# Optimization experiments

Measured on AMD Instinct MI355X. Metric: run time of the kernel, lower is better.

## Reference

```python
import jax, jax.numpy as jnp
import numpy as np

HEAD_DIM = 128
N_HEADS = 16
N_KV_HEADS = 4
N_REP = N_HEADS // N_KV_HEADS


def _rope(x, cos, sin):
    # x: [B, S, Hk, D]; cos/sin: [S, D/2]
    xr = x.reshape(*x.shape[:-1], -1, 2)
    x0, x1 = xr[..., 0], xr[..., 1]
    c = cos[None, :, None, :]
    s = sin[None, :, None, :]
    o0 = x0 * c - x1 * s
    o1 = x0 * s + x1 * c
    return jnp.stack([o0, o1], axis=-1).reshape(x.shape)


def setup_inputs() -> dict:
    key = jax.random.key(0)
    ks = jax.random.split(key, 7)
    B, S, DIM = 2, 1024, 2048
    KV_DIM = HEAD_DIM * N_KV_HEADS
    x = jax.random.normal(ks[0], (B, S, DIM), dtype=jnp.float32)
    # rotary angles like LLaMA: freqs = 1/10000^(2i/D)
    inv_freq = 1.0 / (10000.0 ** (np.arange(0, HEAD_DIM, 2, dtype=np.float32) / HEAD_DIM))
    ang = np.arange(S, dtype=np.float32)[:, None] * inv_freq[None, :]  # [S, D/2]
    theta_cos = jnp.asarray(np.cos(ang))
    theta_sin = jnp.asarray(np.sin(ang))
    sc = 0.02
    wq = jax.random.normal(ks[1], (DIM, DIM), dtype=jnp.float32) * sc
    wk = jax.random.normal(ks[2], (DIM, KV_DIM), dtype=jnp.float32) * sc
    wv = jax.random.normal(ks[3], (DIM, KV_DIM), dtype=jnp.float32) * sc
    wo = jax.random.normal(ks[4], (DIM, DIM), dtype=jnp.float32) * sc
    return {"x": x, "theta_cos": theta_cos, "theta_sin": theta_sin,
            "wq": wq, "wk": wk, "wv": wv, "wo": wo}


def reference(x, theta_cos, theta_sin, wq, wk, wv, wo):
    B, S, DIM = x.shape
    # projections
    xq = (x @ wq).reshape(B, S, N_HEADS, HEAD_DIM).transpose(0, 2, 1, 3)  # [B,H,S,D]
    xk = (x @ wk).reshape(B, S, N_KV_HEADS, HEAD_DIM)                      # [B,S,Hk,D]
    xv = (x @ wv).reshape(B, S, N_KV_HEADS, HEAD_DIM)
    # RoPE on K and V only (faithful to source: Q is NOT rotated)
    xk = _rope(xk, theta_cos, theta_sin)
    xv = _rope(xv, theta_cos, theta_sin)
    # GQA repeat: [B,S,Hk,D] -> [B,H,S,D] (each kv head repeated consecutively)
    xk = jnp.repeat(xk.transpose(0, 2, 1, 3), N_REP, axis=1)
    xv = jnp.repeat(xv.transpose(0, 2, 1, 3), N_REP, axis=1)
    scale = HEAD_DIM ** (-0.5)
    att = jnp.einsum('bhqd,bhkd->bhqk', xq, xk) * scale
    # faithful masking: tril then masked_fill(att == 0, -inf)
    tri = jnp.tril(jnp.ones((S, S), dtype=bool))
    att = jnp.where(tri[None, None], att, 0.0)
    att = jnp.where(att == 0.0, -jnp.inf, att)
    att = jax.nn.softmax(att, axis=-1)
    y = jnp.einsum('bhqk,bhkd->bhqd', att, xv)
    out = y.transpose(0, 2, 1, 3).reshape(B, S, DIM)
    return out @ wo
```

## Files before the change

kernel.cpp:

```cpp
#include <hip/hip_runtime.h>
#include <hip/hip_bf16.h>
#include <stdint.h>
#include <math.h>

typedef _Float16 half_t;
typedef __attribute__((ext_vector_type(2))) _Float16 h2_t;
typedef __attribute__((ext_vector_type(4))) _Float16 h4_t;
typedef __attribute__((ext_vector_type(8))) _Float16 h8_t;
typedef __attribute__((ext_vector_type(4))) float f32x4;
typedef __attribute__((ext_vector_type(4))) uint32_t u32x4;

#if __has_builtin(__builtin_amdgcn_exp2f)
#define EXP2(x) __builtin_amdgcn_exp2f(x)
#else
#define EXP2(x) exp2f(x)
#endif

__device__ __forceinline__ void gload16(const void* g, void* l) {
    __builtin_amdgcn_global_load_lds(
        (const __attribute__((address_space(1))) uint32_t*)(uintptr_t)g,
        (__attribute__((address_space(3))) uint32_t*)(uint32_t)(uintptr_t)l,
        16, 0, 0);
}

__global__ __launch_bounds__(256) void prep(const float* __restrict__ x, half_t* __restrict__ xh,
                                            const float* __restrict__ wq, const float* __restrict__ wk,
                                            const float* __restrict__ wv, const float* __restrict__ wo,
                                            half_t* __restrict__ qt, half_t* __restrict__ kt,
                                            half_t* __restrict__ vt, half_t* __restrict__ ot) {
    __shared__ half_t T[32][36];
    const int bx = blockIdx.x;
    if (bx < 2048) {
        int g = (bx * 256 + threadIdx.x) * 8;
        float4 a = *(const float4*)(x + g);
        float4 b = *(const float4*)(x + g + 4);
        h8_t o = {(half_t)a.x,(half_t)a.y,(half_t)a.z,(half_t)a.w,
                  (half_t)b.x,(half_t)b.y,(half_t)b.z,(half_t)b.w};
        *(h8_t*)(xh + g) = o;
        return;
    }
    const int wb = bx - 2048;
    const float* src; half_t* dst; int Nd, t;
    if (wb < 4096)      { src = wq; dst = qt; Nd = 2048; t = wb; }
    else if (wb < 5120) { src = wk; dst = kt; Nd = 512;  t = wb - 4096; }
    else if (wb < 6144) { src = wv; dst = vt; Nd = 512;  t = wb - 5120; }
    else                { src = wo; dst = ot; Nd = 2048; t = wb - 6144; }
    const int K = 2048;
    int nt = Nd >> 5;
    int ti = t / nt, tj = t % nt;
    int r  = threadIdx.x >> 3;
    int c4 = (threadIdx.x & 7) << 2;
    float4 v = *(const float4*)(src + (size_t)(ti*32 + r) * Nd + tj*32 + c4);
    T[r][c4+0] = (half_t)v.x; T[r][c4+1] = (half_t)v.y;
    T[r][c4+2] = (half_t)v.z; T[r][c4+3] = (half_t)v.w;
    __syncthreads();
    h4_t o = {T[c4+0][r], T[c4+1][r], T[c4+2][r], T[c4+3][r]};
    *(h4_t*)(dst + (size_t)(tj*32 + r) * K + ti*32 + c4) = o;
}

template<int BM, int QKV, typename CT>
__global__ __launch_bounds__(256) void gemm_t(const half_t* __restrict__ A,
                                              const half_t* __restrict__ Bq,
                                              const half_t* __restrict__ Bk,
                                              const half_t* __restrict__ Bv,
                                              CT* __restrict__ Cq,
                                              half_t* __restrict__ Ck,
                                              half_t* __restrict__ Vt,
                                              const float* __restrict__ Cs,
                                              const float* __restrict__ Sn,
                                              int NB, int K) {
    constexpr int MI  = BM / 32;
    constexpr int ACH = BM / 8;
    constexpr int TOT = ACH + 16;
    constexpr int PW  = TOT / 4;
    __shared__ half_t SMEM[BM * 64 + 128 * 64];
    half_t* Ah = SMEM;
    half_t* Bh = SMEM + BM * 64;
    const int tid = threadIdx.x, lane = tid & 63, wid = tid >> 6;
    const int lr = lane & 15, lg = lane >> 4;
    const int wm = wid >> 1, wn = wid & 1;
    const int bid = blockIdx.x;
    const int xcd   = bid & 7;
    const int local = bid >> 3;
    const int perx  = NB >> 3;
    const int bn = perx * xcd + local % perx;
    const int bm = local / perx;
    const int m0 = bm * BM;

    const half_t* W; CT* Cc; int cs, col0;
    if constexpr (QKV) {
        if (bn < 16)      { W = Bq + (size_t)bn * 128 * K;        Cc = Cq;       cs = 2048; col0 = bn * 128; }
        else if (bn < 20) { W = Bk + (size_t)(bn - 16) * 128 * K; Cc = (CT*)Ck;  cs = 512;  col0 = (bn - 16) * 128; }
        else              { W = Bv + (size_t)(bn - 20) * 128 * K; Cc = (CT*)Ck;  cs = 512;  col0 = (bn - 20) * 128; }
    } else {
        W = Bq + (size_t)bn * 128 * K; Cc = Cq; cs = NB * 128; col0 = bn * 128;
    }

    const half_t* Arow = A + (size_t)m0 * K;
    f32x4 acc[MI][4] = {};

    for (int k0 = 0; k0 < K; k0 += 64) {
        #pragma unroll
        for (int c = 0; c < PW; c++) {
            const int chunk = wid * PW + c;
            const int o = lane * 16;
            if (chunk < ACH) {
                const int go   = (chunk << 10) + o;
                const int row  = go >> 7;
                const int colb = (go & 127) ^ ((row & 7) << 4);
                gload16(Arow + (size_t)row * K + k0 + (colb >> 1), (char*)Ah + (chunk << 10));
            } else {
                const int go   = ((chunk - ACH) << 10) + o;
                const int row  = go >> 7;
                const int colb = (go & 127) ^ ((row & 7) << 4);
                gload16(W + (size_t)row * K + k0 + (colb >> 1), (char*)Bh + ((chunk - ACH) << 10));
            }
        }
        __syncthreads();
        h8_t af[2][MI], bf[2][4];
        #pragma unroll
        for (int kk = 0; kk < 2; kk++) {
            #pragma unroll
            for (int mi = 0; mi < MI; mi++) {
                const int row = wm * (BM / 2) + mi * 16 + lr;
                const int cb  = (kk * 64 + lg * 16) ^ ((lr & 7) << 4);
                af[kk][mi] = *(const h8_t*)((const char*)Ah + row * 128 + cb);
            }
            #pragma unroll
            for (int ni = 0; ni < 4; ni++) {
                const int row = wn * 64 + ni * 16 + lr;
                const int cb  = (kk * 64 + lg * 16) ^ ((lr & 7) << 4);
                bf[kk][ni] = *(const h8_t*)((const char*)Bh + row * 128 + cb);
            }
        }
        #pragma unroll
        for (int kk = 0; kk < 2; kk++)
            #pragma unroll
            for (int mi = 0; mi < MI; mi++)
                #pragma unroll
                for (int ni = 0; ni < 4; ni++)
                    acc[mi][ni] = __builtin_amdgcn_mfma_f32_16x16x32_f16(af[kk][mi], bf[kk][ni], acc[mi][ni], 0, 0, 0);
        __syncthreads();
    }

    if constexpr (QKV) {
        if (bn >= 16) {
            #pragma unroll
            for (int ni = 0; ni < 4; ni++) {
                const int dh  = wn * 64 + ni * 16 + lr;
                const int p   = dh >> 1;
                const float sg = (lr & 1) ? 1.f : -1.f;
                #pragma unroll
                for (int mi = 0; mi < MI; mi++)
                    #pragma unroll
                    for (int r = 0; r < 4; r++) {
                        const int row = m0 + wm * (BM / 2) + mi * 16 + lg * 4 + r;
                        const int s = row & 1023;
                        const float c  = Cs[s * 64 + p];
                        const float si = Sn[s * 64 + p];
                        const float own = acc[mi][ni][r];
                        const float par = __shfl_xor(own, 1);
                        acc[mi][ni][r] = own * c + par * (sg * si);
                    }
            }
            if (bn >= 20) {
                __syncthreads();
                half_t* T = SMEM;
                constexpr int LD = 68;
                #pragma unroll
                for (int mi = 0; mi < MI; mi++)
                    #pragma unroll
                    for (int ni = 0; ni < 4; ni++) {
                        const int d  = wn * 64 + ni * 16 + lr;
                        const int s0 = wm * (BM / 2) + mi * 16 + lg * 4;
                        h4_t o = {(half_t)acc[mi][ni][0], (half_t)acc[mi][ni][1],
                                  (half_t)acc[mi][ni][2], (half_t)acc[mi][ni][3]};
                        *(h4_t*)(T + d * LD + s0) = o;
                    }
                __syncthreads();
                #pragma unroll
                for (int it = 0; it < 4; it++) {
                    const int d  = it * 32 + (tid >> 3);
                    const int c8 = (tid & 7) * 8;
                    h8_t o;
                    #pragma unroll
                    for (int e = 0; e < 8; e++) o[e] = T[d * LD + c8 + e];
                    *(h8_t*)(Vt + (size_t)(col0 + d) * 2048 + m0 + c8) = o;
                }
                return;
            }
        }
    }

    #pragma unroll
    for (int mi = 0; mi < MI; mi++)
        #pragma unroll
        for (int ni = 0; ni < 4; ni++)
            #pragma unroll
            for (int r = 0; r < 4; r++) {
                int row = m0 + wm * (BM / 2) + mi * 16 + lg * 4 + r;
                int col = col0 + wn * 64 + ni * 16 + lr;
                Cc[(size_t)row * cs + col] = (CT)acc[mi][ni][r];
            }
}

__global__ __launch_bounds__(256, 3) void attn9(const half_t* __restrict__ Qh,
                                                const half_t* __restrict__ Kh,
                                                const half_t* __restrict__ Vtg,
                                                half_t* __restrict__ Yh,
                                                half_t* __restrict__ Yp,
                                                float* __restrict__ ML) {
    __shared__ half_t K0[64 * 128];
    __shared__ half_t V0[128 * 64];

    const int tid = threadIdx.x, lane = tid & 63, wid = tid >> 6;
    const int lr = lane & 15, lg = lane >> 4;
    const int bx = blockIdx.x;
    const int g  = bx & 7;
    const int local = bx >> 3;
    const int b = g >> 2, kvh = g & 3;
    const int h = kvh * 4 + (local & 3);
    const int pp = local >> 2;
    int qt, kb0, kb1, part; bool partial;
    if (pp < 8)            { qt = 8 + pp;           kb0 = 0; kb1 = 7;  partial = true;  part = 0; }
    else if (!(pp & 1))    { qt = 7 - ((pp-8)>>1);  kb0 = 0; kb1 = qt; partial = false; part = 0; }
    else                   { qt = 15 - ((pp-9)>>1); kb0 = 8; kb1 = qt; partial = true;  part = 1; }

    const int qbase = qt * 64 + wid * 16;
    const int q     = qbase + lr;
    const size_t kbase = (size_t)b * 1024;

    const float sc2 = 0.08838834764831845f * 1.4426950408889634f;
    h8_t qf[4];
    #pragma unroll
    for (int kk = 0; kk < 4; kk++) {
        qf[kk] = *(const h8_t*)(Qh + ((size_t)(b * 1024) + q) * 2048 + h * 128 + kk * 32 + lg * 8);
        qf[kk] = qf[kk] * (half_t)sc2;
    }

    float m = -1e30f, l = 0.f;
    f32x4 yacc[8] = {};

    {
        const int j = kb0 * 64;
        #pragma unroll
        for (int c = 0; c < 4; c++) {
            const int chunk = wid * 4 + c;
            const int o = (chunk << 10) + lane * 16;
            { const int row  = o >> 8;
              const int colb = (o & 255) ^ ((row & 7) << 4);
              gload16(Kh + (kbase + j + row) * 512 + kvh * 128 + (colb >> 1),
                      (char*)K0 + (chunk << 10)); }
            { const int row  = o >> 7;
              const int colb = (o & 127) ^ ((row & 7) << 4);
              gload16(Vtg + (size_t)(kvh * 128 + row) * 2048 + kbase + j + (colb >> 1),
                      (char*)V0 + (chunk << 10)); }
        }
    }
    __syncthreads();

    for (int kb = kb0; kb <= kb1; kb++) {
        const bool pf = (kb + 1 <= kb1);
        h8_t kpre[4], vpre[4];
        if (pf) {
            const int j2 = (kb + 1) * 64;
            #pragma unroll
            for (int c = 0; c < 4; c++) {
                const int chunk = wid * 4 + c;
                const int o = (chunk << 10) + lane * 16;
                { const int row  = o >> 8;
                  const int colb = (o & 255) ^ ((row & 7) << 4);
                  kpre[c] = *(const h8_t*)(Kh + (kbase + j2 + row) * 512 + kvh * 128 + (colb >> 1)); }
                { const int row  = o >> 7;
                  const int colb = (o & 127) ^ ((row & 7) << 4);
                  vpre[c] = *(const h8_t*)(Vtg + (size_t)(kvh * 128 + row) * 2048 + kbase + j2 + (colb >> 1)); }
            }
        }

        const int j = kb * 64;
        f32x4 st[4] = {};
        __builtin_amdgcn_s_setprio(1);
        #pragma unroll
        for (int t4 = 0; t4 < 4; t4++)
            #pragma unroll
            for (int kk = 0; kk < 4; kk++) {
                const int row = t4 * 16 + lr;
                const int cb  = (kk * 64 + lg * 16) ^ ((lr & 7) << 4);
                h8_t kf = *(const h8_t*)((const char*)K0 + row * 256 + cb);
                st[t4] = __builtin_amdgcn_mfma_f32_16x16x32_f16(kf, qf[kk], st[t4], 0, 0, 0);
            }
        __builtin_amdgcn_s_setprio(0);
        if (kb == qt) {
            #pragma unroll
            for (int t4 = 0; t4 < 4; t4++)
                #pragma unroll
                for (int r = 0; r < 4; r++)
                    if (j + t4 * 16 + lg * 4 + r > q) st[t4][r] = -1e30f;
        }
        float mb = fmaxf(fmaxf(fmaxf(st[0][0], st[0][1]), fmaxf(st[0][2], st[0][3])),
                         fmaxf(fmaxf(st[1][0], st[1][1]), fmaxf(st[1][2], st[1][3])));
        mb = fmaxf(mb, fmaxf(fmaxf(fmaxf(st[2][0], st[2][1]), fmaxf(st[2][2], st[2][3])),
                             fmaxf(fmaxf(st[3][0], st[3][1]), fmaxf(st[3][2], st[3][3]))));
        mb = fmaxf(mb, __shfl_xor(mb, 16));
        mb = fmaxf(mb, __shfl_xor(mb, 32));
        if (!__all(mb - m <= 8.0f)) {
            float mn = fmaxf(m, mb);
            float al = EXP2(m - mn);
            m = mn;
            l *= al;
            #pragma unroll
            for (int dt = 0; dt < 8; dt++)
                #pragma unroll
                for (int r = 0; r < 4; r++)
                    yacc[dt][r] *= al;
        }
        float rs = 0.f;
        #pragma unroll
        for (int t4 = 0; t4 < 4; t4++)
            #pragma unroll
            for (int r = 0; r < 4; r++) {
                float p = EXP2(st[t4][r] - m);
                st[t4][r] = p;
                rs += p;
            }
        rs += __shfl_xor(rs, 16);
        rs += __shfl_xor(rs, 32);
        l += rs;
        uint32_t h2p[4][2];
        #pragma unroll
        for (int t4 = 0; t4 < 4; t4++) {
            h2p[t4][0] = __builtin_bit_cast(uint32_t,
                __builtin_amdgcn_cvt_pkrtz(st[t4][0], st[t4][1]));
            h2p[t4][1] = __builtin_bit_cast(uint32_t,
                __builtin_amdgcn_cvt_pkrtz(st[t4][2], st[t4][3]));
        }
        const int src1 = ((lg & 1) << 5) + lr;
        const int src2 = src1 + 16;
        const bool sel = (lg < 2);
        h8_t pb[2];
        #pragma unroll
        for (int c = 0; c < 2; c++) {
            uint32_t lo0 = __shfl((int)h2p[2*c][0],   src1);
            uint32_t lo1 = __shfl((int)h2p[2*c][1],   src1);
            uint32_t lo2 = __shfl((int)h2p[2*c][0],   src2);
            uint32_t lo3 = __shfl((int)h2p[2*c][1],   src2);
            uint32_t hi0 = __shfl((int)h2p[2*c+1][0], src1);
            uint32_t hi1 = __shfl((int)h2p[2*c+1][1], src1);
            uint32_t hi2 = __shfl((int)h2p[2*c+1][0], src2);
            uint32_t hi3 = __shfl((int)h2p[2*c+1][1], src2);
            u32x4 w = { sel ? lo0 : hi0, sel ? lo1 : hi1,
                        sel ? lo2 : hi2, sel ? lo3 : hi3 };
            pb[c] = __builtin_bit_cast(h8_t, w);
        }
        __builtin_amdgcn_s_setprio(1);
        #pragma unroll
        for (int dt = 0; dt < 8; dt++) {
            const int row = dt * 16 + lr;
            const int cb0 = (lg * 16) ^ ((lr & 7) << 4);
            const int cb1 = (64 + lg * 16) ^ ((lr & 7) << 4);
            h8_t v0 = *(const h8_t*)((const char*)V0 + row * 128 + cb0);
            h8_t v1 = *(const h8_t*)((const char*)V0 + row * 128 + cb1);
            yacc[dt] = __builtin_amdgcn_mfma_f32_16x16x32_f16(v0, pb[0], yacc[dt], 0, 0, 0);
            yacc[dt] = __builtin_amdgcn_mfma_f32_16x16x32_f16(v1, pb[1], yacc[dt], 0, 0, 0);
        }
        __builtin_amdgcn_s_setprio(0);

        __syncthreads();
        if (pf) {
            #pragma unroll
            for (int c = 0; c < 4; c++) {
                const int chunk = wid * 4 + c;
                const int o = (chunk << 10) + lane * 16;
                *(h8_t*)((char*)K0 + o) = kpre[c];
                *(h8_t*)((char*)V0 + o) = vpre[c];
            }
            __syncthreads();
        }
    }

    const float inv = 1.0f / l;
    if (!partial) {
        #pragma unroll
        for (int dt = 0; dt < 8; dt++) {
            h4_t o = {(half_t)(yacc[dt][0] * inv), (half_t)(yacc[dt][1] * inv),
                      (half_t)(yacc[dt][2] * inv), (half_t)(yacc[dt][3] * inv)};
            *(h4_t*)(Yh + ((size_t)(b * 1024) + q) * 2048 + h * 128 + dt * 16 + lg * 4) = o;
        }
    } else {
        const int pidx = ((b * 16 + h) * 8 + (qt - 8)) * 2 + part;
        half_t* yp = Yp + (size_t)pidx * 8192;
        const int rl = wid * 16 + lr;
        #pragma unroll
        for (int dt = 0; dt < 8; dt++) {
            h4_t o = {(half_t)(yacc[dt][0] * inv), (half_t)(yacc[dt][1] * inv),
                      (half_t)(yacc[dt][2] * inv), (half_t)(yacc[dt][3] * inv)};
            *(h4_t*)(yp + rl * 128 + dt * 16 + lg * 4) = o;
        }
        if (lg == 0) {
            float* ml = ML + (size_t)pidx * 128;
            ml[rl]      = m;
            ml[64 + rl] = l;
        }
    }
}

__global__ __launch_bounds__(256) void merge2(const half_t* __restrict__ Yp,
                                              const float* __restrict__ ML,
                                              half_t* __restrict__ Yh) {
    const int sidx = blockIdx.x;
    const int b = sidx >> 7;
    const int rem = sidx & 127;
    const int h = rem >> 3;
    const int qt = 8 + (rem & 7);
    const int t = threadIdx.x;
    const int row = t >> 2;
    const int cg = (t & 3) * 32;
    const float* ml0 = ML + (size_t)(sidx * 2) * 128;
    const float* ml1 = ml0 + 128;
    const float m0 = ml0[row], l0 = ml0[64 + row];
    const float m1 = ml1[row], l1 = ml1[64 + row];
    const float M  = fmaxf(m0, m1);
    const float w0 = l0 * EXP2(m0 - M), w1 = l1 * EXP2(m1 - M);
    const float inv = 1.0f / (w0 + w1);
    const float a0 = w0 * inv, a1 = w1 * inv;
    const half_t* y0 = Yp + (size_t)(sidx * 2) * 8192 + row * 128 + cg;
    const half_t* y1 = y0 + 8192;
    half_t* out = Yh + ((size_t)(b * 1024 + qt * 64 + row)) * 2048 + h * 128 + cg;
    #pragma unroll
    for (int c = 0; c < 32; c += 8) {
        h8_t u = *(const h8_t*)(y0 + c);
        h8_t v = *(const h8_t*)(y1 + c);
        h8_t o;
        #pragma unroll
        for (int e = 0; e < 8; e++)
            o[e] = (half_t)(a0 * (float)u[e] + a1 * (float)v[e]);
        *(h8_t*)(out + c) = o;
    }
}

extern "C" void kernel_launch(void* const* d_in, const int* in_sizes, int n_in,
                              void* d_out, int out_size, void* d_ws, size_t ws_size,
                              hipStream_t stream) {
    const float* x  = (const float*)d_in[0];
    const float* tc = (const float*)d_in[1];
    const float* ts = (const float*)d_in[2];
    const float* wq = (const float*)d_in[3];
    const float* wk = (const float*)d_in[4];
    const float* wv = (const float*)d_in[5];
    const float* wo = (const float*)d_in[6];
    float* out = (float*)d_out;

    const size_t MD = 2048ull * 2048, MK = 2048ull * 512;
    half_t* Xh  = (half_t*)d_ws;
    half_t* Qh  = Xh  + MD;
    half_t* Kh  = Qh  + MD;
    half_t* Vh  = Kh  + MK;
    half_t* Vt  = Vh  + MK;
    half_t* Yh  = Vt  + MK;
    half_t* wqt = Yh  + MD;
    half_t* wkt = wqt + MD;
    half_t* wvt = wkt + MK;
    half_t* wot = wvt + MK;
    half_t* Yp  = wot + MD;
    float*  ML  = (float*)(Yp + 512ull * 8192);

    prep<<<12288, 256, 0, stream>>>(x, Xh, wq, wk, wv, wo, wqt, wkt, wvt, wot);
    gemm_t<64, 1, half_t><<<768, 256, 0, stream>>>(Xh, wqt, wkt, wvt, Qh, Kh, Vt, tc, ts, 24, 2048);
    attn9<<<768, 256, 0, stream>>>(Qh, Kh, Vt, Yh, Yp, ML);
    merge2<<<256, 256, 0, stream>>>(Yp, ML, Yh);
    gemm_t<64, 0, float><<<512, 256, 0, stream>>>(Yh, wot, nullptr, nullptr, out, nullptr, nullptr, nullptr, nullptr, 16, 2048);
}
```

Before: 109.5 us.

## Double-buffer LDS tiles in GEMM to overlap global loads with MFMA

The GEMM kernel now keeps two LDS stage buffers and issues the async global-to-LDS loads for the next K tile before computing on the current one. This halves the barriers per K step and lets memory latency hide behind MFMA work. In exchange it doubles shared memory use to 48KB per block, which may lower occupancy. BM is fixed to 64 and the template parameter is dropped.

```diff
diff --git a/kernel.cpp b/kernel.cpp
--- a/kernel.cpp
+++ b/kernel.cpp
@@ -58,7 +58,7 @@
     *(h4_t*)(dst + (size_t)(tj*32 + r) * K + ti*32 + c4) = o;
 }
 
-template<int BM, int QKV, typename CT>
+template<int QKV, typename CT>
 __global__ __launch_bounds__(256) void gemm_t(const half_t* __restrict__ A,
                                               const half_t* __restrict__ Bq,
                                               const half_t* __restrict__ Bk,
@@ -69,13 +69,15 @@
                                               const float* __restrict__ Cs,
                                               const float* __restrict__ Sn,
                                               int NB, int K) {
-    constexpr int MI  = BM / 32;
-    constexpr int ACH = BM / 8;
-    constexpr int TOT = ACH + 16;
-    constexpr int PW  = TOT / 4;
-    __shared__ half_t SMEM[BM * 64 + 128 * 64];
-    half_t* Ah = SMEM;
-    half_t* Bh = SMEM + BM * 64;
+    constexpr int BM  = 64;
+    constexpr int MI  = 2;
+    constexpr int ACH = 8;
+    constexpr int PW  = 6;
+    __shared__ half_t SMEM[2 * (64 + 128) * 64];
+    half_t* A0 = SMEM;
+    half_t* B0 = SMEM + 64 * 64;
+    half_t* A1 = SMEM + 192 * 64;
+    half_t* B1 = A1 + 64 * 64;
     const int tid = threadIdx.x, lane = tid & 63, wid = tid >> 6;
     const int lr = lane & 15, lg = lane >> 4;
     const int wm = wid >> 1, wn = wid & 1;
@@ -99,7 +101,7 @@
     const half_t* Arow = A + (size_t)m0 * K;
     f32x4 acc[MI][4] = {};
 
-    for (int k0 = 0; k0 < K; k0 += 64) {
+    auto stage = [&](half_t* Ah, half_t* Bh, int k0) {
         #pragma unroll
         for (int c = 0; c < PW; c++) {
             const int chunk = wid * PW + c;
@@ -116,13 +118,15 @@
                 gload16(W + (size_t)row * K + k0 + (colb >> 1), (char*)Bh + ((chunk - ACH) << 10));
             }
         }
-        __syncthreads();
+    };
+
+    auto compute = [&](const half_t* Ah, const half_t* Bh) {
         h8_t af[2][MI], bf[2][4];
         #pragma unroll
         for (int kk = 0; kk < 2; kk++) {
             #pragma unroll
             for (int mi = 0; mi < MI; mi++) {
-                const int row = wm * (BM / 2) + mi * 16 + lr;
+                const int row = wm * 32 + mi * 16 + lr;
                 const int cb  = (kk * 64 + lg * 16) ^ ((lr & 7) << 4);
                 af[kk][mi] = *(const h8_t*)((const char*)Ah + row * 128 + cb);
             }
@@ -140,6 +144,16 @@
                 #pragma unroll
                 for (int ni = 0; ni < 4; ni++)
                     acc[mi][ni] = __builtin_amdgcn_mfma_f32_16x16x32_f16(af[kk][mi], bf[kk][ni], acc[mi][ni], 0, 0, 0);
+    };
+
+    stage(A0, B0, 0);
+    __syncthreads();
+    for (int k0 = 0; k0 < K; k0 += 128) {
+        stage(A1, B1, k0 + 64);
+        compute(A0, B0);
+        __syncthreads();
+        if (k0 + 128 < K) stage(A0, B0, k0 + 128);
+        compute(A1, B1);
         __syncthreads();
     }
 
@@ -154,7 +168,7 @@
                 for (int mi = 0; mi < MI; mi++)
                     #pragma unroll
                     for (int r = 0; r < 4; r++) {
-                        const int row = m0 + wm * (BM / 2) + mi * 16 + lg * 4 + r;
+                        const int row = m0 + wm * 32 + mi * 16 + lg * 4 + r;
                         const int s = row & 1023;
                         const float c  = Cs[s * 64 + p];
                         const float si = Sn[s * 64 + p];
@@ -172,7 +186,7 @@
                     #pragma unroll
                     for (int ni = 0; ni < 4; ni++) {
                         const int d  = wn * 64 + ni * 16 + lr;
-                        const int s0 = wm * (BM / 2) + mi * 16 + lg * 4;
+                        const int s0 = wm * 32 + mi * 16 + lg * 4;
                         h4_t o = {(half_t)acc[mi][ni][0], (half_t)acc[mi][ni][1],
                                   (half_t)acc[mi][ni][2], (half_t)acc[mi][ni][3]};
                         *(h4_t*)(T + d * LD + s0) = o;
@@ -198,7 +212,7 @@
         for (int ni = 0; ni < 4; ni++)
             #pragma unroll
             for (int r = 0; r < 4; r++) {
-                int row = m0 + wm * (BM / 2) + mi * 16 + lg * 4 + r;
+                int row = m0 + wm * 32 + mi * 16 + lg * 4 + r;
                 int col = col0 + wn * 64 + ni * 16 + lr;
                 Cc[(size_t)row * cs + col] = (CT)acc[mi][ni][r];
             }
@@ -465,8 +479,8 @@
     float*  ML  = (float*)(Yp + 512ull * 8192);
 
     prep<<<12288, 256, 0, stream>>>(x, Xh, wq, wk, wv, wo, wqt, wkt, wvt, wot);
-    gemm_t<64, 1, half_t><<<768, 256, 0, stream>>>(Xh, wqt, wkt, wvt, Qh, Kh, Vt, tc, ts, 24, 2048);
+    gemm_t<1, half_t><<<768, 256, 0, stream>>>(Xh, wqt, wkt, wvt, Qh, Kh, Vt, tc, ts, 24, 2048);
     attn9<<<768, 256, 0, stream>>>(Qh, Kh, Vt, Yh, Yp, ML);
     merge2<<<256, 256, 0, stream>>>(Yp, ML, Yh);
-    gemm_t<64, 0, float><<<512, 256, 0, stream>>>(Yh, wot, nullptr, nullptr, out, nullptr, nullptr, nullptr, nullptr, 16, 2048);
-}
+    gemm_t<0, float><<<512, 256, 0, stream>>>(Yh, wot, nullptr, nullptr, out, nullptr, nullptr, nullptr, nullptr, 16, 2048);
+}
```

Result: faster. 103.3 us (-5.7%).
